# Performance work log

Hardware: AMD Instinct MI355X
Metric: run time of the kernel (lower is better)

## Reference

```python
import jax, jax.numpy as jnp
import numpy as np

B, S, F, D, H, L, K = 64, 512, 8, 512, 8, 2, 512
FF = 4 * D
DH = D // H


def _ln(x):
    m = jnp.mean(x, axis=-1, keepdims=True)
    v = jnp.var(x, axis=-1, keepdims=True)
    return (x - m) * jax.lax.rsqrt(v + 1e-5)


def _encoder_layer(x, Wqkv, Wo, W1, b1, W2, b2):
    # pre-LN multi-head self-attention
    h = _ln(x)
    qkv = h @ Wqkv                                   # [B,S,3D]
    q, k, v = jnp.split(qkv, 3, axis=-1)
    q = q.reshape(B, S, H, DH)
    k = k.reshape(B, S, H, DH)
    v = v.reshape(B, S, H, DH)
    scores = jnp.einsum('bqhd,bkhd->bhqk', q, k) / jnp.sqrt(jnp.float32(DH))
    attn = jax.nn.softmax(scores, axis=-1)
    o = jnp.einsum('bhqk,bkhd->bqhd', attn, v).reshape(B, S, D) @ Wo
    x = x + o
    # pre-LN feed-forward
    h = _ln(x)
    x = x + (jax.nn.relu(h @ W1 + b1) @ W2 + b2)
    return x


def setup_inputs() -> dict:
    key = jax.random.key(0)
    ks = jax.random.split(key, 12)
    sc = 0.02
    inp = {
        'x': jax.random.normal(ks[0], (B, S, F), dtype=jnp.float32),
        'enc_W': jax.random.normal(ks[1], (F, D), dtype=jnp.float32) * sc,
        'enc_b': jnp.zeros((D,), dtype=jnp.float32),
        'Wqkv': jax.random.normal(ks[2], (L, D, 3 * D), dtype=jnp.float32) * sc,
        'Wo': jax.random.normal(ks[3], (L, D, D), dtype=jnp.float32) * sc,
        'W1': jax.random.normal(ks[4], (L, D, FF), dtype=jnp.float32) * sc,
        'b1': jnp.zeros((L, FF), dtype=jnp.float32),
        'W2': jax.random.normal(ks[5], (L, FF, D), dtype=jnp.float32) * sc,
        'b2': jnp.zeros((L, D), dtype=jnp.float32),
        'centers': jax.random.normal(ks[6], (K, D), dtype=jnp.float32),
    }
    return inp


def reference(x, enc_W, enc_b, Wqkv, Wo, W1, b1, W2, b2, centers):
    # enc_embedding
    h = x @ enc_W + enc_b                            # [B,S,D]
    # seq_model: stack of standard transformer encoder layers
    for i in range(L):
        h = _encoder_layer(h, Wqkv[i], Wo[i], W1[i], b1[i], W2[i], b2[i])
    output_seq = h                                   # [B,S,D]
    # torch.cdist(output_seq, centers, p=2) via matmul expansion
    on2 = jnp.sum(output_seq * output_seq, axis=-1, keepdims=True)   # [B,S,1]
    cn2 = jnp.sum(centers * centers, axis=-1)                        # [K]
    dist2 = on2 + cn2[None, None, :] - 2.0 * jnp.einsum('bsd,kd->bsk', output_seq, centers)
    cluster_ids = jnp.argmin(dist2, axis=-1)                         # [B,S]
    assigned_centroids = centers[cluster_ids]                        # [B,S,D] gather
    diff = output_seq - assigned_centroids
    # torch.norm(diff, dim=1)**2 then mean == mean over (B,D) of sum over S of diff^2
    loss = jnp.mean(jnp.sum(diff * diff, axis=1))
    return loss, output_seq
```

## Files before the change

### kernel.cpp

```cpp
#include <hip/hip_runtime.h>
#include <cstdint>
#include <cstddef>

typedef __attribute__((ext_vector_type(4))) float f32x4;
typedef __attribute__((ext_vector_type(8))) short s16x8;
typedef __attribute__((ext_vector_type(4))) short s16x4;

__device__ __forceinline__ short f2bf(float f){
  unsigned u; __builtin_memcpy(&u, &f, 4);
  u += 0x7fffu + ((u >> 16) & 1u);
  return (short)(u >> 16);
}

__device__ __forceinline__ void gll16(const void* g, void* l) {
  auto* lp = (__attribute__((address_space(3))) unsigned*)(uintptr_t)(l);
  const auto* gp = (const __attribute__((address_space(1))) unsigned*)(uintptr_t)(g);
  __builtin_amdgcn_global_load_lds(gp, lp, 16, 0, 0);
}

__device__ __forceinline__ void ds_tr8(unsigned a, s16x4* r) {
  asm volatile(
    "ds_read_b64_tr_b16 %0, %8\n\t"
    "ds_read_b64_tr_b16 %1, %8 offset:512\n\t"
    "ds_read_b64_tr_b16 %2, %8 offset:2048\n\t"
    "ds_read_b64_tr_b16 %3, %8 offset:2560\n\t"
    "ds_read_b64_tr_b16 %4, %8 offset:4096\n\t"
    "ds_read_b64_tr_b16 %5, %8 offset:4608\n\t"
    "ds_read_b64_tr_b16 %6, %8 offset:6144\n\t"
    "ds_read_b64_tr_b16 %7, %8 offset:6656\n\t"
    "s_waitcnt lgkmcnt(0)"
    : "=&v"(r[0]), "=&v"(r[1]), "=&v"(r[2]), "=&v"(r[3]),
      "=&v"(r[4]), "=&v"(r[5]), "=&v"(r[6]), "=&v"(r[7])
    : "v"(a)
    : "memory");
}

__global__ __launch_bounds__(256) void encode_kernel(
    const float* __restrict__ x, const float* __restrict__ W,
    const float* __restrict__ b, float* __restrict__ out)
{
  const int t = blockIdx.x;
  float xv[8];
#pragma unroll
  for (int f = 0; f < 8; ++f) xv[f] = x[(size_t)t*8 + f];
  for (int d = threadIdx.x; d < 512; d += 256) {
    float acc = b[d];
#pragma unroll
    for (int f = 0; f < 8; ++f) acc += xv[f] * W[f*512 + d];
    out[(size_t)t*512 + d] = acc;
  }
}

__global__ __launch_bounds__(256) void ln_kernel(
    const float* __restrict__ x, short* __restrict__ out)
{
  const int w = threadIdx.x >> 6, lane = threadIdx.x & 63;
  const int t = blockIdx.x * 4 + w;
  const float* row = x + (size_t)t * 512;
  float4 v0 = *(const float4*)&row[lane*8];
  float4 v1 = *(const float4*)&row[lane*8 + 4];
  float vals[8] = {v0.x,v0.y,v0.z,v0.w,v1.x,v1.y,v1.z,v1.w};
  float s = 0.f, sq = 0.f;
#pragma unroll
  for (int i = 0; i < 8; ++i) { s += vals[i]; sq += vals[i]*vals[i]; }
#pragma unroll
  for (int m = 1; m < 64; m <<= 1) { s += __shfl_xor(s, m); sq += __shfl_xor(sq, m); }
  float mean = s * (1.f/512.f);
  float var  = sq * (1.f/512.f) - mean*mean;
  float rstd = rsqrtf(var + 1e-5f);
  s16x8 o;
#pragma unroll
  for (int i = 0; i < 8; ++i) o[i] = f2bf((vals[i]-mean)*rstd);
  *(s16x8*)&out[(size_t)t*512 + lane*8] = o;
}

__global__ __launch_bounds__(256) void packB_kernel(
    const float* __restrict__ in, short* __restrict__ out, int K, int N)
{
  const int n = blockIdx.x * 256 + threadIdx.x;
  const int k = blockIdx.y;
  const int ntk = K >> 5;
  const int idx = ((n >> 4) * ntk + (k >> 5)) * 512 + (((k >> 3) & 3) * 16 + (n & 15)) * 8 + (k & 7);
  out[idx] = f2bf(in[(size_t)k * N + n]);
}

__global__ __launch_bounds__(256) void packBNK_kernel(
    const float* __restrict__ in, short* __restrict__ out, int K, int N)
{
  const int k = blockIdx.x * 256 + threadIdx.x;
  const int n = blockIdx.y;
  const int ntk = K >> 5;
  const int idx = ((n >> 4) * ntk + (k >> 5)) * 512 + (((k >> 3) & 3) * 16 + (n & 15)) * 8 + (k & 7);
  out[idx] = f2bf(in[(size_t)n * K + k]);
}

template<bool BIAS, bool RELU, bool RESID, bool OUT32>
__global__ __launch_bounds__(512, 1) void gemm_kernel(
    const short* __restrict__ A, const short* __restrict__ Bp,
    void* Cout, const float* __restrict__ bias,
    const float* resid, int M, int N, int K)
{
  __shared__ short As[4][256 * 32];
  const int tid = threadIdx.x;
  const int lane = tid & 63, w = tid >> 6;
  const int wr = w >> 2, wc = w & 3;
  const int q = lane & 15, g = lane >> 4;

  const int nx = gridDim.x;
  const int d = blockIdx.y * nx + blockIdx.x;
  const int per = (nx * gridDim.y) >> 3;
  const int lid = (d & 7) * per + (d >> 3);
  const int bx = lid % nx, by = lid / nx;
  const int m0 = by * 256, n0 = bx * 256;

  const int srow = lane >> 2;
  const int scol = (((lane & 3) ^ ((lane >> 4) & 3)) * 8);
  const short* aS0 = A + (size_t)(m0 + w*32 + srow) * K + scol;
  const short* aS1 = aS0 + (size_t)16 * K;
  const int d0 = (w*2) * 512, d1 = (w*2 + 1) * 512;

  const int gs = (g ^ (q >> 2)) * 8;

  const int nt = K >> 5;
  const size_t bstep = (size_t)nt * 512;
  const short* bp0 = Bp + ((size_t)(n0 >> 4) + wc * 4) * bstep + lane * 8;

  f32x4 acc[8][4] = {};

  auto STAGE_A = [&](int tt) {
    const int k0 = tt << 5, nb = tt & 3;
    gll16(aS0 + k0, &As[nb][d0]);
    gll16(aS1 + k0, &As[nb][d1]);
  };
  s16x8 bA[4], bB[4];
  auto LOADB = [&](int tt, s16x8* bf) {
#pragma unroll
    for (int i = 0; i < 4; ++i)
      bf[i] = *(const s16x8*)&bp0[(size_t)i * bstep + (size_t)tt * 512];
  };
  auto TILE = [&](int t, s16x8* bcur, s16x8* bnxt, bool doLB, bool doSA) {
    __builtin_amdgcn_s_barrier();
    __builtin_amdgcn_sched_barrier(0);
    if (doLB) LOADB(t + 1, bnxt);
    __builtin_amdgcn_sched_barrier(0);
    if (doSA) STAGE_A(t + 3);
    __builtin_amdgcn_sched_barrier(0);
    const short* Ab = &As[t & 3][0];
    s16x8 aF[8];
#pragma unroll
    for (int i = 0; i < 8; ++i) aF[i] = *(const s16x8*)&Ab[(wr*128 + i*16 + q)*32 + gs];
    __builtin_amdgcn_s_setprio(1);
#pragma unroll
    for (int mi = 0; mi < 8; ++mi)
#pragma unroll
      for (int ni = 0; ni < 4; ++ni)
        acc[mi][ni] = __builtin_amdgcn_mfma_f32_16x16x32_bf16(aF[mi], bcur[ni], acc[mi][ni], 0, 0, 0);
    __builtin_amdgcn_s_setprio(0);
  };

  STAGE_A(0);
  LOADB(0, bA);
  STAGE_A(1);
  STAGE_A(2);

  for (int t = 0; t < nt - 2; t += 2) {
    asm volatile("s_waitcnt vmcnt(8)" ::: "memory");
    TILE(t, bA, bB, true, true);
    asm volatile("s_waitcnt vmcnt(8)" ::: "memory");
    TILE(t + 1, bB, bA, true, t + 4 < nt);
  }
  asm volatile("s_waitcnt vmcnt(6)" ::: "memory");
  TILE(nt - 2, bA, bB, true, false);
  asm volatile("s_waitcnt vmcnt(4)" ::: "memory");
  TILE(nt - 1, bB, bA, false, false);

#pragma unroll
  for (int mi = 0; mi < 8; ++mi) {
#pragma unroll
    for (int r = 0; r < 4; ++r) {
      const int gr = m0 + wr*128 + mi*16 + g*4 + r;
#pragma unroll
      for (int ni = 0; ni < 4; ++ni) {
        const int gc = n0 + wc*64 + ni*16 + q;
        float v = acc[mi][ni][r];
        if (BIAS) v += bias[gc];
        if (RELU) v = fmaxf(v, 0.f);
        if (RESID) v += resid[(size_t)gr * N + gc];
        if (OUT32) ((float*)Cout)[(size_t)gr * N + gc] = v;
        else       ((short*)Cout)[(size_t)gr * N + gc] = f2bf(v);
      }
    }
  }
}

__global__ __launch_bounds__(256) void attn_kernel(
    const short* __restrict__ qkv, short* __restrict__ attn_out)
{
  __shared__ short Ks[2][64 * 64];
  __shared__ short Vs[2][64 * 64];
  const int tid = threadIdx.x;
  const int w = tid >> 6, lane = tid & 63;
  const int q16 = lane & 15, g = lane >> 4;
  const int dd = blockIdx.x;
  const int lid = (dd & 7) * (int)(gridDim.x >> 3) + (dd >> 3);
  const int qt4 = lid & 7, h = (lid >> 3) & 7, b = lid >> 6;
  const size_t base = (size_t)b * 512 * 1536;
  const int qrow = qt4*64 + w*16 + q16;

  s16x8 bQ0, bQ1;
  {
    const size_t p = base + (size_t)qrow * 1536 + h*64 + g*8;
    bQ0 = *(const s16x8*)&qkv[p];
    bQ1 = *(const s16x8*)&qkv[p + 32];
  }

  const int c0 = w*2, c1 = w*2 + 1;
  const short* kS0 = qkv + base + (size_t)(c0*8 + (lane>>3))*1536 + 512 + h*64 + ((lane&7)^(lane>>3))*8;
  const short* kS1 = qkv + base + (size_t)(c1*8 + (lane>>3))*1536 + 512 + h*64 + ((lane&7)^(lane>>3))*8;
  const short* vS0 = qkv + base + (size_t)((c0&1)*32 + (lane>>1))*1536 + 1024 + h*64 + (c0>>1)*16 + (lane&1)*8;
  const short* vS1 = qkv + base + (size_t)((c1&1)*32 + (lane>>1))*1536 + 1024 + h*64 + (c1>>1)*16 + (lane&1)*8;

  const unsigned vs_lane = (unsigned)(size_t)(&Vs[0][0]) + (unsigned)((q16 + g*64)*2);
  const int sw = q16 & 7;

  float mrun = -1e30f, ssum = 0.f;
  f32x4 O[4] = {};

  gll16(kS0, &Ks[0][c0*512]);
  gll16(kS1, &Ks[0][c1*512]);
  gll16(vS0, &Vs[0][c0*512]);
  gll16(vS1, &Vs[0][c1*512]);
  __syncthreads();

  int cur = 0;
  for (int j0 = 0; j0 < 512; j0 += 64) {
    s16x8 ka0[4], ka1[4];
#pragma unroll
    for (int grp = 0; grp < 4; ++grp) {
      const int rb = (grp*16 + q16) * 64;
      ka0[grp] = *(const s16x8*)&Ks[cur][rb + ((g    ) ^ sw)*8];
      ka1[grp] = *(const s16x8*)&Ks[cur][rb + ((g + 4) ^ sw)*8];
    }
    if (j0 + 64 < 512) {
      const size_t joff = (size_t)(j0 + 64) * 1536;
      const int nxt = cur ^ 1;
      gll16(kS0 + joff, &Ks[nxt][c0*512]);
      gll16(kS1 + joff, &Ks[nxt][c1*512]);
      gll16(vS0 + joff, &Vs[nxt][c0*512]);
      gll16(vS1 + joff, &Vs[nxt][c1*512]);
    }
    __builtin_amdgcn_sched_barrier(0);

    f32x4 c[4];
    __builtin_amdgcn_s_setprio(1);
#pragma unroll
    for (int grp = 0; grp < 4; ++grp) {
      f32x4 z = {};
      c[grp] = __builtin_amdgcn_mfma_f32_16x16x32_bf16(ka0[grp], bQ0, z, 0, 0, 0);
      c[grp] = __builtin_amdgcn_mfma_f32_16x16x32_bf16(ka1[grp], bQ1, c[grp], 0, 0, 0);
    }
    __builtin_amdgcn_s_setprio(0);

    float sc[16];
#pragma unroll
    for (int grp = 0; grp < 4; ++grp)
#pragma unroll
      for (int r = 0; r < 4; ++r) sc[grp*4 + r] = c[grp][r] * 0.125f;
    float bm = sc[0];
#pragma unroll
    for (int i = 1; i < 16; ++i) bm = fmaxf(bm, sc[i]);
    bm = fmaxf(bm, __shfl_xor(bm, 16));
    bm = fmaxf(bm, __shfl_xor(bm, 32));
    const float mn = fmaxf(mrun, bm);
    const float alpha = __expf(mrun - mn);
    float p[16]; float bs = 0.f;
#pragma unroll
    for (int i = 0; i < 16; ++i) { p[i] = __expf(sc[i] - mn); bs += p[i]; }
    bs += __shfl_xor(bs, 16);
    bs += __shfl_xor(bs, 32);
    ssum = ssum * alpha + bs;
    mrun = mn;
#pragma unroll
    for (int db = 0; db < 4; ++db) O[db] *= alpha;

#pragma unroll
    for (int kk = 0; kk < 2; ++kk) {
      s16x8 pf;
#pragma unroll
      for (int e = 0; e < 8; ++e) pf[e] = f2bf(p[(kk*2 + (e >> 2))*4 + (e & 3)]);
      s16x4 r[8];
      ds_tr8(vs_lane + (unsigned)(cur << 13) + (unsigned)(kk*1024), r);
      __builtin_amdgcn_sched_barrier(0);
      __builtin_amdgcn_s_setprio(1);
#pragma unroll
      for (int db = 0; db < 4; ++db) {
        s16x8 vf = __builtin_shufflevector(r[2*db], r[2*db + 1], 0, 1, 2, 3, 4, 5, 6, 7);
        O[db] = __builtin_amdgcn_mfma_f32_16x16x32_bf16(vf, pf, O[db], 0, 0, 0);
      }
      __builtin_amdgcn_s_setprio(0);
    }
    __syncthreads();
    cur ^= 1;
  }

  const float inv = 1.f / ssum;
  const size_t tok = (size_t)b*512 + qrow;
#pragma unroll
  for (int db = 0; db < 4; ++db) {
    s16x4 ov;
#pragma unroll
    for (int r = 0; r < 4; ++r) ov[r] = f2bf(O[db][r] * inv);
    *(s16x4*)&attn_out[tok*512 + h*64 + db*16 + g*4] = ov;
  }
}

__global__ __launch_bounds__(256) void finalize_seq_kernel(
    const float* __restrict__ resid, float* __restrict__ outseq, short* __restrict__ obf)
{
  const size_t i = (size_t)blockIdx.x * 256 + threadIdx.x;
  const float v = resid[i];
  outseq[i] = v;
  obf[i] = f2bf(v);
}

__global__ __launch_bounds__(256) void cn2_kernel(
    const float* __restrict__ centers, float* __restrict__ cn2)
{
  const int c = blockIdx.x;
  __shared__ float red[256];
  float s = 0.f;
  for (int d = threadIdx.x; d < 512; d += 256) { float v = centers[(size_t)c*512 + d]; s += v*v; }
  red[threadIdx.x] = s; __syncthreads();
  for (int off = 128; off > 0; off >>= 1) {
    if (threadIdx.x < off) red[threadIdx.x] += red[threadIdx.x + off];
    __syncthreads();
  }
  if (threadIdx.x == 0) cn2[c] = red[0];
}

__global__ __launch_bounds__(256) void argmin_kernel(
    const float* __restrict__ gdist, const float* __restrict__ cn2,
    const float* __restrict__ resid, const float* __restrict__ centers,
    float* __restrict__ partial)
{
  const int w = threadIdx.x >> 6, lane = threadIdx.x & 63;
  const int t = blockIdx.x * 4 + w;
  float best = 1e30f; int bi = 0;
#pragma unroll
  for (int j = 0; j < 8; ++j) {
    const int k = j*64 + lane;
    const float v = cn2[k] - 2.f * gdist[(size_t)t*512 + k];
    if (v < best || (v == best && k < bi)) { best = v; bi = k; }
  }
#pragma unroll
  for (int mm = 1; mm < 64; mm <<= 1) {
    const float ov = __shfl_xor(best, mm); const int oi = __shfl_xor(bi, mm);
    if (ov < best || (ov == best && oi < bi)) { best = ov; bi = oi; }
  }
  float s = 0.f;
#pragma unroll
  for (int j = 0; j < 2; ++j) {
    float4 o = *(const float4*)&resid[(size_t)t*512 + lane*8 + j*4];
    float4 c = *(const float4*)&centers[(size_t)bi*512 + lane*8 + j*4];
    const float dx = o.x-c.x, dy = o.y-c.y, dz = o.z-c.z, dw = o.w-c.w;
    s += dx*dx + dy*dy + dz*dz + dw*dw;
  }
#pragma unroll
  for (int mm = 1; mm < 64; mm <<= 1) s += __shfl_xor(s, mm);
  __shared__ float red[4];
  if (lane == 0) red[w] = s;
  __syncthreads();
  if (threadIdx.x == 0) partial[blockIdx.x] = red[0] + red[1] + red[2] + red[3];
}

__global__ __launch_bounds__(256) void loss_kernel(
    const float* __restrict__ partial, int n, float* __restrict__ out)
{
  float s = 0.f;
  for (int i = threadIdx.x; i < n; i += 256) s += partial[i];
  __shared__ float red[256];
  red[threadIdx.x] = s; __syncthreads();
  for (int off = 128; off > 0; off >>= 1) {
    if (threadIdx.x < off) red[threadIdx.x] += red[threadIdx.x + off];
    __syncthreads();
  }
  if (threadIdx.x == 0) out[0] = red[0] * (1.f / 32768.f);
}

extern "C" void kernel_launch(void* const* d_in, const int* in_sizes, int n_in,
                              void* d_out, int out_size, void* d_ws, size_t ws_size,
                              hipStream_t stream) {
  const float* x     = (const float*)d_in[0];
  const float* enc_W = (const float*)d_in[1];
  const float* enc_b = (const float*)d_in[2];
  const float* Wqkv  = (const float*)d_in[3];
  const float* Wo    = (const float*)d_in[4];
  const float* W1    = (const float*)d_in[5];
  const float* b1    = (const float*)d_in[6];
  const float* W2    = (const float*)d_in[7];
  const float* b2    = (const float*)d_in[8];
  const float* cen   = (const float*)d_in[9];
  float* out = (float*)d_out;

  const int NT = 32768;
  char* ws = (char*)d_ws;
  float* resid   = (float*)(ws);
  short* h_ln    = (short*)(ws + 67108864);
  char*  pool    = ws + 100663296;
  short* qkv     = (short*)pool;
  short* attn_o  = (short*)(pool + 100663296);
  short* hidden  = (short*)pool;
  float* gdist   = (float*)pool;
  short* wbase   = (short*)(ws + 234881024);
  short* wqT     = wbase;
  short* woT     = wbase + 1572864;
  short* w1T     = wbase + 2097152;
  short* w2T     = wbase + 4194304;
  short* cenb    = wbase + 6291456;
  float* cn2     = (float*)(ws + 247988224);
  float* partial = (float*)(ws + 247990272);

  for (int l = 0; l < 2; ++l) {
    packB_kernel<<<dim3(6, 512), 256, 0, stream>>>(Wqkv + (size_t)l*512*1536, wqT + (size_t)l*786432, 512, 1536);
    packB_kernel<<<dim3(2, 512), 256, 0, stream>>>(Wo   + (size_t)l*512*512,  woT + (size_t)l*262144, 512, 512);
    packB_kernel<<<dim3(8, 512), 256, 0, stream>>>(W1   + (size_t)l*512*2048, w1T + (size_t)l*1048576, 512, 2048);
    packB_kernel<<<dim3(2, 2048), 256, 0, stream>>>(W2  + (size_t)l*2048*512, w2T + (size_t)l*1048576, 2048, 512);
  }
  packBNK_kernel<<<dim3(2, 512), 256, 0, stream>>>(cen, cenb, 512, 512);
  cn2_kernel<<<512, 256, 0, stream>>>(cen, cn2);

  encode_kernel<<<NT, 256, 0, stream>>>(x, enc_W, enc_b, resid);

  for (int l = 0; l < 2; ++l) {
    ln_kernel<<<NT/4, 256, 0, stream>>>(resid, h_ln);
    gemm_kernel<false,false,false,false><<<dim3(6, 128), 512, 0, stream>>>(
        h_ln, wqT + (size_t)l*786432, qkv, nullptr, nullptr, NT, 1536, 512);
    attn_kernel<<<4096, 256, 0, stream>>>(qkv, attn_o);
    gemm_kernel<false,false,true,true><<<dim3(2, 128), 512, 0, stream>>>(
        attn_o, woT + (size_t)l*262144, resid, nullptr, resid, NT, 512, 512);
    ln_kernel<<<NT/4, 256, 0, stream>>>(resid, h_ln);
    gemm_kernel<true,true,false,false><<<dim3(8, 128), 512, 0, stream>>>(
        h_ln, w1T + (size_t)l*1048576, hidden, b1 + (size_t)l*2048, nullptr, NT, 2048, 512);
    gemm_kernel<true,false,true,true><<<dim3(2, 128), 512, 0, stream>>>(
        hidden, w2T + (size_t)l*1048576, resid, b2 + (size_t)l*512, resid, NT, 512, 2048);
  }

  finalize_seq_kernel<<<65536, 256, 0, stream>>>(resid, out + 1, h_ln);
  gemm_kernel<false,false,false,true><<<dim3(2, 128), 512, 0, stream>>>(
      h_ln, cenb, gdist, nullptr, nullptr, NT, 512, 512);
  argmin_kernel<<<NT/4, 256, 0, stream>>>(gdist, cn2, resid, cen, partial);
  loss_kernel<<<1, 256, 0, stream>>>(partial, NT/4, out);
}
```

Measured before the change: 935.7 us.

## Stage B through LDS for narrow GEMMs and fuse final output write

Measured after the change: 920.6 us. Within noise of the previous version (-1.6%).

```diff
diff --git a/kernel.cpp b/kernel.cpp
--- a/kernel.cpp
+++ b/kernel.cpp
@@ -74,6 +74,21 @@
   *(s16x8*)&out[(size_t)t*512 + lane*8] = o;
 }
 
+__global__ __launch_bounds__(256) void transpose_bf16_kernel(
+    const float* __restrict__ in, short* __restrict__ out, int K, int N, int kshift)
+{
+  const int o = blockIdx.x * 256 + threadIdx.x;
+  const int k = o & (K - 1), n = o >> kshift;
+  out[o] = f2bf(in[(size_t)k * N + n]);
+}
+
+__global__ __launch_bounds__(256) void convert_bf16_kernel(
+    const float* __restrict__ in, short* __restrict__ out)
+{
+  const int i = blockIdx.x * 256 + threadIdx.x;
+  out[i] = f2bf(in[i]);
+}
+
 __global__ __launch_bounds__(256) void packB_kernel(
     const float* __restrict__ in, short* __restrict__ out, int K, int N)
 {
@@ -84,23 +99,14 @@
   out[idx] = f2bf(in[(size_t)k * N + n]);
 }
 
-__global__ __launch_bounds__(256) void packBNK_kernel(
-    const float* __restrict__ in, short* __restrict__ out, int K, int N)
-{
-  const int k = blockIdx.x * 256 + threadIdx.x;
-  const int n = blockIdx.y;
-  const int ntk = K >> 5;
-  const int idx = ((n >> 4) * ntk + (k >> 5)) * 512 + (((k >> 3) & 3) * 16 + (n & 15)) * 8 + (k & 7);
-  out[idx] = f2bf(in[(size_t)n * K + k]);
-}
-
-template<bool BIAS, bool RELU, bool RESID, bool OUT32>
-__global__ __launch_bounds__(512, 1) void gemm_kernel(
-    const short* __restrict__ A, const short* __restrict__ Bp,
+template<bool BIAS, bool RELU, bool RESID, bool OUT32, bool FINAL>
+__global__ __launch_bounds__(512, 1) void gemm_ldsb_kernel(
+    const short* __restrict__ A, const short* __restrict__ Bt,
     void* Cout, const float* __restrict__ bias,
-    const float* resid, int M, int N, int K)
+    const float* resid, short* __restrict__ obf, int M, int N, int K)
 {
   __shared__ short As[4][256 * 32];
+  __shared__ short Bs[4][256 * 32];
   const int tid = threadIdx.x;
   const int lane = tid & 63, w = tid >> 6;
   const int wr = w >> 2, wc = w & 3;
@@ -115,10 +121,101 @@
 
   const int srow = lane >> 2;
   const int scol = (((lane & 3) ^ ((lane >> 4) & 3)) * 8);
+  const short* aS0 = A  + (size_t)(m0 + w*32 + srow) * K + scol;
+  const short* aS1 = aS0 + (size_t)16 * K;
+  const short* bS0 = Bt + (size_t)(n0 + w*32 + srow) * K + scol;
+  const short* bS1 = bS0 + (size_t)16 * K;
+  const int d0 = (w*2) * 512, d1 = (w*2 + 1) * 512;
+  const int gs = (g ^ (q >> 2)) * 8;
+
+  f32x4 acc[8][4] = {};
+  const int nt = K >> 5;
+
+  auto STAGE = [&](int tt) {
+    const int k0 = tt << 5, nb = tt & 3;
+    gll16(aS0 + k0, &As[nb][d0]);
+    gll16(aS1 + k0, &As[nb][d1]);
+    gll16(bS0 + k0, &Bs[nb][d0]);
+    gll16(bS1 + k0, &Bs[nb][d1]);
+  };
+  auto COMPUTE = [&](int t) {
+    const int bufc = t & 3;
+    if (t + 3 < nt) STAGE(t + 3);
+    s16x8 aF[8], bF[4];
+#pragma unroll
+    for (int i = 0; i < 8; ++i) aF[i] = *(const s16x8*)&As[bufc][(wr*128 + i*16 + q)*32 + gs];
+#pragma unroll
+    for (int i = 0; i < 4; ++i) bF[i] = *(const s16x8*)&Bs[bufc][(wc*64 + i*16 + q)*32 + gs];
+#pragma unroll
+    for (int mi = 0; mi < 8; ++mi)
+#pragma unroll
+      for (int ni = 0; ni < 4; ++ni)
+        acc[mi][ni] = __builtin_amdgcn_mfma_f32_16x16x32_bf16(aF[mi], bF[ni], acc[mi][ni], 0, 0, 0);
+  };
+
+  STAGE(0); STAGE(1); STAGE(2);
+
+  for (int t = 0; t < nt - 2; ++t) {
+    asm volatile("s_waitcnt vmcnt(8)" ::: "memory");
+    __builtin_amdgcn_s_barrier();
+    __builtin_amdgcn_sched_barrier(0);
+    COMPUTE(t);
+    __builtin_amdgcn_sched_barrier(0);
+  }
+  asm volatile("s_waitcnt vmcnt(4)" ::: "memory");
+  __builtin_amdgcn_s_barrier();
+  __builtin_amdgcn_sched_barrier(0);
+  COMPUTE(nt - 2);
+  asm volatile("s_waitcnt vmcnt(0)" ::: "memory");
+  __builtin_amdgcn_s_barrier();
+  __builtin_amdgcn_sched_barrier(0);
+  COMPUTE(nt - 1);
+
+#pragma unroll
+  for (int mi = 0; mi < 8; ++mi) {
+#pragma unroll
+    for (int r = 0; r < 4; ++r) {
+      const int gr = m0 + wr*128 + mi*16 + g*4 + r;
+#pragma unroll
+      for (int ni = 0; ni < 4; ++ni) {
+        const int gc = n0 + wc*64 + ni*16 + q;
+        float v = acc[mi][ni][r];
+        if (BIAS) v += bias[gc];
+        if (RELU) v = fmaxf(v, 0.f);
+        if (RESID) v += resid[(size_t)gr * N + gc];
+        const size_t idx = (size_t)gr * N + gc;
+        if (FINAL) { ((float*)Cout)[idx] = v; obf[idx] = f2bf(v); }
+        else if (OUT32) ((float*)Cout)[idx] = v;
+        else ((short*)Cout)[idx] = f2bf(v);
+      }
+    }
+  }
+}
+
+template<bool BIAS, bool RELU, bool RESID, bool OUT32>
+__global__ __launch_bounds__(512, 1) void gemm_regb_kernel(
+    const short* __restrict__ A, const short* __restrict__ Bp,
+    void* Cout, const float* __restrict__ bias,
+    const float* resid, int M, int N, int K)
+{
+  __shared__ short As[4][256 * 32];
+  const int tid = threadIdx.x;
+  const int lane = tid & 63, w = tid >> 6;
+  const int wr = w >> 2, wc = w & 3;
+  const int q = lane & 15, g = lane >> 4;
+
+  const int nx = gridDim.x;
+  const int d = blockIdx.y * nx + blockIdx.x;
+  const int per = (nx * gridDim.y) >> 3;
+  const int lid = (d & 7) * per + (d >> 3);
+  const int bx = lid % nx, by = lid / nx;
+  const int m0 = by * 256, n0 = bx * 256;
+
+  const int srow = lane >> 2;
+  const int scol = (((lane & 3) ^ ((lane >> 4) & 3)) * 8);
   const short* aS0 = A + (size_t)(m0 + w*32 + srow) * K + scol;
   const short* aS1 = aS0 + (size_t)16 * K;
   const int d0 = (w*2) * 512, d1 = (w*2 + 1) * 512;
-
   const int gs = (g ^ (q >> 2)) * 8;
 
   const int nt = K >> 5;
@@ -314,15 +411,6 @@
   }
 }
 
-__global__ __launch_bounds__(256) void finalize_seq_kernel(
-    const float* __restrict__ resid, float* __restrict__ outseq, short* __restrict__ obf)
-{
-  const size_t i = (size_t)blockIdx.x * 256 + threadIdx.x;
-  const float v = resid[i];
-  outseq[i] = v;
-  obf[i] = f2bf(v);
-}
-
 __global__ __launch_bounds__(256) void cn2_kernel(
     const float* __restrict__ centers, float* __restrict__ cn2)
 {
@@ -340,7 +428,7 @@
 
 __global__ __launch_bounds__(256) void argmin_kernel(
     const float* __restrict__ gdist, const float* __restrict__ cn2,
-    const float* __restrict__ resid, const float* __restrict__ centers,
+    const float* __restrict__ seq, const float* __restrict__ centers,
     float* __restrict__ partial)
 {
   const int w = threadIdx.x >> 6, lane = threadIdx.x & 63;
@@ -359,11 +447,12 @@
   }
   float s = 0.f;
 #pragma unroll
-  for (int j = 0; j < 2; ++j) {
-    float4 o = *(const float4*)&resid[(size_t)t*512 + lane*8 + j*4];
-    float4 c = *(const float4*)&centers[(size_t)bi*512 + lane*8 + j*4];
-    const float dx = o.x-c.x, dy = o.y-c.y, dz = o.z-c.z, dw = o.w-c.w;
-    s += dx*dx + dy*dy + dz*dz + dw*dw;
+  for (int j = 0; j < 8; ++j) {
+    const int dcol = j*64 + lane;
+    const float o = seq[(size_t)t*512 + dcol];
+    const float c = centers[(size_t)bi*512 + dcol];
+    const float dv = o - c;
+    s += dv * dv;
   }
 #pragma unroll
   for (int mm = 1; mm < 64; mm <<= 1) s += __shfl_xor(s, mm);
@@ -412,42 +501,46 @@
   short* hidden  = (short*)pool;
   float* gdist   = (float*)pool;
   short* wbase   = (short*)(ws + 234881024);
-  short* wqT     = wbase;
+  short* wqP     = wbase;
   short* woT     = wbase + 1572864;
-  short* w1T     = wbase + 2097152;
+  short* w1P     = wbase + 2097152;
   short* w2T     = wbase + 4194304;
   short* cenb    = wbase + 6291456;
   float* cn2     = (float*)(ws + 247988224);
   float* partial = (float*)(ws + 247990272);
 
   for (int l = 0; l < 2; ++l) {
-    packB_kernel<<<dim3(6, 512), 256, 0, stream>>>(Wqkv + (size_t)l*512*1536, wqT + (size_t)l*786432, 512, 1536);
-    packB_kernel<<<dim3(2, 512), 256, 0, stream>>>(Wo   + (size_t)l*512*512,  woT + (size_t)l*262144, 512, 512);
-    packB_kernel<<<dim3(8, 512), 256, 0, stream>>>(W1   + (size_t)l*512*2048, w1T + (size_t)l*1048576, 512, 2048);
-    packB_kernel<<<dim3(2, 2048), 256, 0, stream>>>(W2  + (size_t)l*2048*512, w2T + (size_t)l*1048576, 2048, 512);
-  }
-  packBNK_kernel<<<dim3(2, 512), 256, 0, stream>>>(cen, cenb, 512, 512);
+    packB_kernel<<<dim3(6, 512), 256, 0, stream>>>(Wqkv + (size_t)l*512*1536, wqP + (size_t)l*786432, 512, 1536);
+    transpose_bf16_kernel<<<1024, 256, 0, stream>>>(Wo  + (size_t)l*512*512,  woT + (size_t)l*262144, 512, 512, 9);
+    packB_kernel<<<dim3(8, 512), 256, 0, stream>>>(W1   + (size_t)l*512*2048, w1P + (size_t)l*1048576, 512, 2048);
+    transpose_bf16_kernel<<<4096, 256, 0, stream>>>(W2  + (size_t)l*2048*512, w2T + (size_t)l*1048576, 2048, 512, 11);
+  }
+  convert_bf16_kernel<<<1024, 256, 0, stream>>>(cen, cenb);
   cn2_kernel<<<512, 256, 0, stream>>>(cen, cn2);
 
   encode_kernel<<<NT, 256, 0, stream>>>(x, enc_W, enc_b, resid);
 
   for (int l = 0; l < 2; ++l) {
     ln_kernel<<<NT/4, 256, 0, stream>>>(resid, h_ln);
-    gemm_kernel<false,false,false,false><<<dim3(6, 128), 512, 0, stream>>>(
-        h_ln, wqT + (size_t)l*786432, qkv, nullptr, nullptr, NT, 1536, 512);
+    gemm_regb_kernel<false,false,false,false><<<dim3(6, 128), 512, 0, stream>>>(
+        h_ln, wqP + (size_t)l*786432, qkv, nullptr, nullptr, NT, 1536, 512);
     attn_kernel<<<4096, 256, 0, stream>>>(qkv, attn_o);
-    gemm_kernel<false,false,true,true><<<dim3(2, 128), 512, 0, stream>>>(
-        attn_o, woT + (size_t)l*262144, resid, nullptr, resid, NT, 512, 512);
+    gemm_ldsb_kernel<false,false,true,true,false><<<dim3(2, 128), 512, 0, stream>>>(
+        attn_o, woT + (size_t)l*262144, resid, nullptr, resid, nullptr, NT, 512, 512);
     ln_kernel<<<NT/4, 256, 0, stream>>>(resid, h_ln);
-    gemm_kernel<true,true,false,false><<<dim3(8, 128), 512, 0, stream>>>(
-        h_ln, w1T + (size_t)l*1048576, hidden, b1 + (size_t)l*2048, nullptr, NT, 2048, 512);
-    gemm_kernel<true,false,true,true><<<dim3(2, 128), 512, 0, stream>>>(
-        hidden, w2T + (size_t)l*1048576, resid, b2 + (size_t)l*512, resid, NT, 512, 2048);
-  }
-
-  finalize_seq_kernel<<<65536, 256, 0, stream>>>(resid, out + 1, h_ln);
-  gemm_kernel<false,false,false,true><<<dim3(2, 128), 512, 0, stream>>>(
-      h_ln, cenb, gdist, nullptr, nullptr, NT, 512, 512);
-  argmin_kernel<<<NT/4, 256, 0, stream>>>(gdist, cn2, resid, cen, partial);
+    gemm_regb_kernel<true,true,false,false><<<dim3(8, 128), 512, 0, stream>>>(
+        h_ln, w1P + (size_t)l*1048576, hidden, b1 + (size_t)l*2048, nullptr, NT, 2048, 512);
+    if (l == 0) {
+      gemm_ldsb_kernel<true,false,true,true,false><<<dim3(2, 128), 512, 0, stream>>>(
+          hidden, w2T + (size_t)l*1048576, resid, b2 + (size_t)l*512, resid, nullptr, NT, 512, 2048);
+    } else {
+      gemm_ldsb_kernel<true,false,true,true,true><<<dim3(2, 128), 512, 0, stream>>>(
+          hidden, w2T + (size_t)l*1048576, out + 1, b2 + (size_t)l*512, resid, h_ln, NT, 512, 2048);
+    }
+  }
+
+  gemm_ldsb_kernel<false,false,false,true,false><<<dim3(2, 128), 512, 0, stream>>>(
+      h_ln, cenb, gdist, nullptr, nullptr, nullptr, NT, 512, 512);
+  argmin_kernel<<<NT/4, 256, 0, stream>>>(gdist, cn2, out + 1, cen, partial);
   loss_kernel<<<1, 256, 0, stream>>>(partial, NT/4, out);
 }
```

## Store GEMM A-operands in pre-packed MFMA tile layout and fuse final copy

Applied to the files above, without the earlier changes.

New measurement: 934.6 us. No clear change (-0.1%).

```diff
diff --git a/kernel.cpp b/kernel.cpp
--- a/kernel.cpp
+++ b/kernel.cpp
@@ -35,6 +35,10 @@
     : "memory");
 }
 
+__device__ __forceinline__ int pidx(int m, int k, int ntk) {
+  return ((m >> 4) * ntk + (k >> 5)) * 512 + ((((k >> 3) & 3) * 16 + (m & 15)) << 3) + (k & 7);
+}
+
 __global__ __launch_bounds__(256) void encode_kernel(
     const float* __restrict__ x, const float* __restrict__ W,
     const float* __restrict__ b, float* __restrict__ out)
@@ -71,7 +75,7 @@
   s16x8 o;
 #pragma unroll
   for (int i = 0; i < 8; ++i) o[i] = f2bf((vals[i]-mean)*rstd);
-  *(s16x8*)&out[(size_t)t*512 + lane*8] = o;
+  *(s16x8*)&out[pidx(t, lane*8, 16)] = o;
 }
 
 __global__ __launch_bounds__(256) void packB_kernel(
@@ -79,9 +83,7 @@
 {
   const int n = blockIdx.x * 256 + threadIdx.x;
   const int k = blockIdx.y;
-  const int ntk = K >> 5;
-  const int idx = ((n >> 4) * ntk + (k >> 5)) * 512 + (((k >> 3) & 3) * 16 + (n & 15)) * 8 + (k & 7);
-  out[idx] = f2bf(in[(size_t)k * N + n]);
+  out[pidx(n, k, K >> 5)] = f2bf(in[(size_t)k * N + n]);
 }
 
 __global__ __launch_bounds__(256) void packBNK_kernel(
@@ -89,18 +91,16 @@
 {
   const int k = blockIdx.x * 256 + threadIdx.x;
   const int n = blockIdx.y;
-  const int ntk = K >> 5;
-  const int idx = ((n >> 4) * ntk + (k >> 5)) * 512 + (((k >> 3) & 3) * 16 + (n & 15)) * 8 + (k & 7);
-  out[idx] = f2bf(in[(size_t)n * K + k]);
-}
-
-template<bool BIAS, bool RELU, bool RESID, bool OUT32>
+  out[pidx(n, k, K >> 5)] = f2bf(in[(size_t)n * K + k]);
+}
+
+template<bool BIAS, bool RELU, bool RESID, int OUTMODE>
 __global__ __launch_bounds__(512, 1) void gemm_kernel(
-    const short* __restrict__ A, const short* __restrict__ Bp,
+    const short* __restrict__ Ap, const short* __restrict__ Bp,
     void* Cout, const float* __restrict__ bias,
-    const float* resid, int M, int N, int K)
-{
-  __shared__ short As[4][256 * 32];
+    const float* resid, short* __restrict__ obf, int M, int N, int K)
+{
+  __shared__ short As[4][16 * 512];
   const int tid = threadIdx.x;
   const int lane = tid & 63, w = tid >> 6;
   const int wr = w >> 2, wc = w & 3;
@@ -113,30 +113,24 @@
   const int bx = lid % nx, by = lid / nx;
   const int m0 = by * 256, n0 = bx * 256;
 
-  const int srow = lane >> 2;
-  const int scol = (((lane & 3) ^ ((lane >> 4) & 3)) * 8);
-  const short* aS0 = A + (size_t)(m0 + w*32 + srow) * K + scol;
-  const short* aS1 = aS0 + (size_t)16 * K;
-  const int d0 = (w*2) * 512, d1 = (w*2 + 1) * 512;
-
-  const int gs = (g ^ (q >> 2)) * 8;
-
   const int nt = K >> 5;
-  const size_t bstep = (size_t)nt * 512;
-  const short* bp0 = Bp + ((size_t)(n0 >> 4) + wc * 4) * bstep + lane * 8;
+  const size_t pstride = (size_t)nt * 512;
+
+  const short* aP = Ap + ((size_t)(m0 >> 4) + w) * pstride + lane * 8;
+  const short* bp0 = Bp + ((size_t)(n0 >> 4) + wc * 4) * pstride + lane * 8;
 
   f32x4 acc[8][4] = {};
 
   auto STAGE_A = [&](int tt) {
-    const int k0 = tt << 5, nb = tt & 3;
-    gll16(aS0 + k0, &As[nb][d0]);
-    gll16(aS1 + k0, &As[nb][d1]);
+    const int nb = tt & 3;
+    gll16(aP + (size_t)tt * 512,               &As[nb][w * 512]);
+    gll16(aP + 8 * pstride + (size_t)tt * 512, &As[nb][(8 + w) * 512]);
   };
   s16x8 bA[4], bB[4];
   auto LOADB = [&](int tt, s16x8* bf) {
 #pragma unroll
     for (int i = 0; i < 4; ++i)
-      bf[i] = *(const s16x8*)&bp0[(size_t)i * bstep + (size_t)tt * 512];
+      bf[i] = *(const s16x8*)&bp0[(size_t)i * pstride + (size_t)tt * 512];
   };
   auto TILE = [&](int t, s16x8* bcur, s16x8* bnxt, bool doLB, bool doSA) {
     __builtin_amdgcn_s_barrier();
@@ -148,7 +142,7 @@
     const short* Ab = &As[t & 3][0];
     s16x8 aF[8];
 #pragma unroll
-    for (int i = 0; i < 8; ++i) aF[i] = *(const s16x8*)&Ab[(wr*128 + i*16 + q)*32 + gs];
+    for (int i = 0; i < 8; ++i) aF[i] = *(const s16x8*)&Ab[(wr*8 + i)*512 + lane*8];
     __builtin_amdgcn_s_setprio(1);
 #pragma unroll
     for (int mi = 0; mi < 8; ++mi)
@@ -174,6 +168,7 @@
   asm volatile("s_waitcnt vmcnt(4)" ::: "memory");
   TILE(nt - 1, bB, bA, false, false);
 
+  const int ntk_out = N >> 5;
 #pragma unroll
   for (int mi = 0; mi < 8; ++mi) {
 #pragma unroll
@@ -186,8 +181,10 @@
         if (BIAS) v += bias[gc];
         if (RELU) v = fmaxf(v, 0.f);
         if (RESID) v += resid[(size_t)gr * N + gc];
-        if (OUT32) ((float*)Cout)[(size_t)gr * N + gc] = v;
-        else       ((short*)Cout)[(size_t)gr * N + gc] = f2bf(v);
+        if (OUTMODE == 0)      ((short*)Cout)[(size_t)gr * N + gc] = f2bf(v);
+        else if (OUTMODE == 1) ((short*)Cout)[pidx(gr, gc, ntk_out)] = f2bf(v);
+        else if (OUTMODE == 2) ((float*)Cout)[(size_t)gr * N + gc] = v;
+        else { ((float*)Cout)[(size_t)gr * N + gc] = v; obf[pidx(gr, gc, ntk_out)] = f2bf(v); }
       }
     }
   }
@@ -304,23 +301,15 @@
   }
 
   const float inv = 1.f / ssum;
-  const size_t tok = (size_t)b*512 + qrow;
+  const int tok = b*512 + qrow;
 #pragma unroll
   for (int db = 0; db < 4; ++db) {
     s16x4 ov;
 #pragma unroll
     for (int r = 0; r < 4; ++r) ov[r] = f2bf(O[db][r] * inv);
-    *(s16x4*)&attn_out[tok*512 + h*64 + db*16 + g*4] = ov;
-  }
-}
-
-__global__ __launch_bounds__(256) void finalize_seq_kernel(
-    const float* __restrict__ resid, float* __restrict__ outseq, short* __restrict__ obf)
-{
-  const size_t i = (size_t)blockIdx.x * 256 + threadIdx.x;
-  const float v = resid[i];
-  outseq[i] = v;
-  obf[i] = f2bf(v);
+    const int d0 = h*64 + db*16 + g*4;
+    *(s16x4*)&attn_out[pidx(tok, d0, 16)] = ov;
+  }
 }
 
 __global__ __launch_bounds__(256) void cn2_kernel(
@@ -340,7 +329,7 @@
 
 __global__ __launch_bounds__(256) void argmin_kernel(
     const float* __restrict__ gdist, const float* __restrict__ cn2,
-    const float* __restrict__ resid, const float* __restrict__ centers,
+    const float* __restrict__ seq, const float* __restrict__ centers,
     float* __restrict__ partial)
 {
   const int w = threadIdx.x >> 6, lane = threadIdx.x & 63;
@@ -359,11 +348,12 @@
   }
   float s = 0.f;
 #pragma unroll
-  for (int j = 0; j < 2; ++j) {
-    float4 o = *(const float4*)&resid[(size_t)t*512 + lane*8 + j*4];
-    float4 c = *(const float4*)&centers[(size_t)bi*512 + lane*8 + j*4];
-    const float dx = o.x-c.x, dy = o.y-c.y, dz = o.z-c.z, dw = o.w-c.w;
-    s += dx*dx + dy*dy + dz*dz + dw*dw;
+  for (int j = 0; j < 8; ++j) {
+    const int dcol = j*64 + lane;
+    const float o = seq[(size_t)t*512 + dcol];
+    const float c = centers[(size_t)bi*512 + dcol];
+    const float dv = o - c;
+    s += dv * dv;
   }
 #pragma unroll
   for (int mm = 1; mm < 64; mm <<= 1) s += __shfl_xor(s, mm);
@@ -412,19 +402,19 @@
   short* hidden  = (short*)pool;
   float* gdist   = (float*)pool;
   short* wbase   = (short*)(ws + 234881024);
-  short* wqT     = wbase;
-  short* woT     = wbase + 1572864;
-  short* w1T     = wbase + 2097152;
-  short* w2T     = wbase + 4194304;
+  short* wqP     = wbase;
+  short* woP     = wbase + 1572864;
+  short* w1P     = wbase + 2097152;
+  short* w2P     = wbase + 4194304;
   short* cenb    = wbase + 6291456;
   float* cn2     = (float*)(ws + 247988224);
   float* partial = (float*)(ws + 247990272);
 
   for (int l = 0; l < 2; ++l) {
-    packB_kernel<<<dim3(6, 512), 256, 0, stream>>>(Wqkv + (size_t)l*512*1536, wqT + (size_t)l*786432, 512, 1536);
-    packB_kernel<<<dim3(2, 512), 256, 0, stream>>>(Wo   + (size_t)l*512*512,  woT + (size_t)l*262144, 512, 512);
-    packB_kernel<<<dim3(8, 512), 256, 0, stream>>>(W1   + (size_t)l*512*2048, w1T + (size_t)l*1048576, 512, 2048);
-    packB_kernel<<<dim3(2, 2048), 256, 0, stream>>>(W2  + (size_t)l*2048*512, w2T + (size_t)l*1048576, 2048, 512);
+    packB_kernel<<<dim3(6, 512), 256, 0, stream>>>(Wqkv + (size_t)l*512*1536, wqP + (size_t)l*786432, 512, 1536);
+    packB_kernel<<<dim3(2, 512), 256, 0, stream>>>(Wo   + (size_t)l*512*512,  woP + (size_t)l*262144, 512, 512);
+    packB_kernel<<<dim3(8, 512), 256, 0, stream>>>(W1   + (size_t)l*512*2048, w1P + (size_t)l*1048576, 512, 2048);
+    packB_kernel<<<dim3(2, 2048), 256, 0, stream>>>(W2  + (size_t)l*2048*512, w2P + (size_t)l*1048576, 2048, 512);
   }
   packBNK_kernel<<<dim3(2, 512), 256, 0, stream>>>(cen, cenb, 512, 512);
   cn2_kernel<<<512, 256, 0, stream>>>(cen, cn2);
@@ -433,21 +423,25 @@
 
   for (int l = 0; l < 2; ++l) {
     ln_kernel<<<NT/4, 256, 0, stream>>>(resid, h_ln);
-    gemm_kernel<false,false,false,false><<<dim3(6, 128), 512, 0, stream>>>(
-        h_ln, wqT + (size_t)l*786432, qkv, nullptr, nullptr, NT, 1536, 512);
+    gemm_kernel<false,false,false,0><<<dim3(6, 128), 512, 0, stream>>>(
+        h_ln, wqP + (size_t)l*786432, qkv, nullptr, nullptr, nullptr, NT, 1536, 512);
     attn_kernel<<<4096, 256, 0, stream>>>(qkv, attn_o);
-    gemm_kernel<false,false,true,true><<<dim3(2, 128), 512, 0, stream>>>(
-        attn_o, woT + (size_t)l*262144, resid, nullptr, resid, NT, 512, 512);
+    gemm_kernel<false,false,true,2><<<dim3(2, 128), 512, 0, stream>>>(
+        attn_o, woP + (size_t)l*262144, resid, nullptr, resid, nullptr, NT, 512, 512);
     ln_kernel<<<NT/4, 256, 0, stream>>>(resid, h_ln);
-    gemm_kernel<true,true,false,false><<<dim3(8, 128), 512, 0, stream>>>(
-        h_ln, w1T + (size_t)l*1048576, hidden, b1 + (size_t)l*2048, nullptr, NT, 2048, 512);
-    gemm_kernel<true,false,true,true><<<dim3(2, 128), 512, 0, stream>>>(
-        hidden, w2T + (size_t)l*1048576, resid, b2 + (size_t)l*512, resid, NT, 512, 2048);
-  }
-
-  finalize_seq_kernel<<<65536, 256, 0, stream>>>(resid, out + 1, h_ln);
-  gemm_kernel<false,false,false,true><<<dim3(2, 128), 512, 0, stream>>>(
-      h_ln, cenb, gdist, nullptr, nullptr, NT, 512, 512);
-  argmin_kernel<<<NT/4, 256, 0, stream>>>(gdist, cn2, resid, cen, partial);
+    gemm_kernel<true,true,false,1><<<dim3(8, 128), 512, 0, stream>>>(
+        h_ln, w1P + (size_t)l*1048576, hidden, b1 + (size_t)l*2048, nullptr, nullptr, NT, 2048, 512);
+    if (l == 0) {
+      gemm_kernel<true,false,true,2><<<dim3(2, 128), 512, 0, stream>>>(
+          hidden, w2P + (size_t)l*1048576, resid, b2 + (size_t)l*512, resid, nullptr, NT, 512, 2048);
+    } else {
+      gemm_kernel<true,false,true,3><<<dim3(2, 128), 512, 0, stream>>>(
+          hidden, w2P + (size_t)l*1048576, out + 1, b2 + (size_t)l*512, resid, h_ln, NT, 512, 2048);
+    }
+  }
+
+  gemm_kernel<false,false,false,2><<<dim3(2, 128), 512, 0, stream>>>(
+      h_ln, cenb, gdist, nullptr, nullptr, nullptr, NT, 512, 512);
+  argmin_kernel<<<NT/4, 256, 0, stream>>>(gdist, cn2, out + 1, cen, partial);
   loss_kernel<<<1, 256, 0, stream>>>(partial, NT/4, out);
 }
```
